# Kernel optimization log

Measured on AMD Instinct MI355X. Metric: run time of the kernel, lower is better.

The kernel has to match this reference:

```python
import jax, jax.numpy as jnp
import numpy as np

D_MODEL = 1024
NUM_HEADS = 16
D_K = D_MODEL // NUM_HEADS


def setup_inputs() -> dict:
    key = jax.random.key(0)
    ks = jax.random.split(key, 11)
    B, T = 4, 2048
    s = 1.0 / np.sqrt(D_MODEL)
    inp = {
        "query": jax.random.normal(ks[0], (B, T, D_MODEL), jnp.float32),
        "key": jax.random.normal(ks[1], (B, T, D_MODEL), jnp.float32),
        "value": jax.random.normal(ks[2], (B, T, D_MODEL), jnp.float32),
        "Wq": jax.random.uniform(ks[3], (D_MODEL, D_MODEL), jnp.float32, -s, s),
        "bq": jax.random.uniform(ks[4], (D_MODEL,), jnp.float32, -s, s),
        "Wk": jax.random.uniform(ks[5], (D_MODEL, D_MODEL), jnp.float32, -s, s),
        "bk": jax.random.uniform(ks[6], (D_MODEL,), jnp.float32, -s, s),
        "Wv": jax.random.uniform(ks[7], (D_MODEL, D_MODEL), jnp.float32, -s, s),
        "bv": jax.random.uniform(ks[8], (D_MODEL,), jnp.float32, -s, s),
        "Wo": jax.random.uniform(ks[9], (D_MODEL, D_MODEL), jnp.float32, -s, s),
        "bo": jax.random.uniform(ks[10], (D_MODEL,), jnp.float32, -s, s),
    }
    return inp


def _split_heads(x):
    B, T, _ = x.shape
    return x.reshape(B, T, NUM_HEADS, D_K).transpose(0, 2, 1, 3)  # (B,H,T,dk)


def reference(query, key, value, Wq, bq, Wk, bk, Wv, bv, Wo, bo):
    q = _split_heads(query @ Wq + bq)   # (B,H,Tq,dk)
    k = _split_heads(key @ Wk + bk)     # (B,H,Tk,dk)
    v = _split_heads(value @ Wv + bv)   # (B,H,Tk,dk)
    scale = 1.0 / jnp.sqrt(jnp.asarray(D_K, q.dtype))
    scores = jnp.einsum("bhqd,bhkd->bhqk", q, k) * scale
    weights = jax.nn.softmax(scores, axis=-1)
    attn = jnp.einsum("bhqk,bhkd->bhqd", weights, v)  # (B,H,Tq,dk)
    B, H, T, dk = attn.shape
    attn = attn.transpose(0, 2, 1, 3).reshape(B, T, H * dk)
    return attn @ Wo + bo
```

## Files before the change

### kernel.cpp

```cpp
#include <hip/hip_runtime.h>
#include <hip/hip_bf16.h>
#include <stdint.h>


typedef __bf16 bf16x8 __attribute__((ext_vector_type(8)));
typedef short  v4s    __attribute__((ext_vector_type(4)));
typedef float  f32x4  __attribute__((ext_vector_type(4)));

#define LOG2E 1.44269504088896340736f

static __device__ __forceinline__ uint32_t f2bf(float x) {
  uint32_t u = __float_as_uint(x);
  u += 0x7fffu + ((u >> 16) & 1u);
  return u >> 16;
}
#if __has_builtin(__builtin_amdgcn_cvt_pk_bf16_f32)
static __device__ __forceinline__ uint32_t pk2bf(float a, float b) {
  typedef __bf16 b2 __attribute__((ext_vector_type(2)));
  union { b2 v; uint32_t u; } x;
  x.v = __builtin_amdgcn_cvt_pk_bf16_f32(a, b);
  return x.u;
}
#else
static __device__ __forceinline__ uint32_t pk2bf(float a, float b) {
  return f2bf(a) | (f2bf(b) << 16);
}
#endif
static __device__ __forceinline__ void gl2lds16(const void* g, void* l) {
  __builtin_amdgcn_global_load_lds(
      (const __attribute__((address_space(1))) uint32_t*)g,
      (__attribute__((address_space(3))) uint32_t*)l, 16, 0, 0);
}

__global__ void convert_inputs(const float* __restrict__ q, const float* __restrict__ k,
                               const float* __restrict__ v, uint16_t* __restrict__ qo,
                               uint16_t* __restrict__ ko, uint16_t* __restrict__ vo) {
  const float* src = blockIdx.y == 0 ? q : (blockIdx.y == 1 ? k : v);
  uint16_t*    dst = blockIdx.y == 0 ? qo : (blockIdx.y == 1 ? ko : vo);
  size_t idx = ((size_t)blockIdx.x * 256 + threadIdx.x) * 8;
  float4 a = *(const float4*)(src + idx);
  float4 b = *(const float4*)(src + idx + 4);
  uint4 o;
  o.x = pk2bf(a.x, a.y); o.y = pk2bf(a.z, a.w);
  o.z = pk2bf(b.x, b.y); o.w = pk2bf(b.z, b.w);
  *(uint4*)(dst + idx) = o;
}

__global__ void transpose_weights(const float* __restrict__ Wq, const float* __restrict__ Wk,
                                  const float* __restrict__ Wv, const float* __restrict__ Wo,
                                  uint16_t* __restrict__ out) {
  __shared__ float t[32][33];
  const float* W = blockIdx.z == 0 ? Wq : blockIdx.z == 1 ? Wk : blockIdx.z == 2 ? Wv : Wo;
  uint16_t* O = out + (size_t)blockIdx.z * 1048576;
  int tx = threadIdx.x & 31, ty = threadIdx.x >> 5;
  int r0 = blockIdx.y * 32, c0 = blockIdx.x * 32;
#pragma unroll
  for (int i = 0; i < 4; i++) t[ty + i * 8][tx] = W[(size_t)(r0 + ty + i * 8) * 1024 + c0 + tx];
  __syncthreads();
#pragma unroll
  for (int i = 0; i < 4; i++)
    O[(size_t)(c0 + ty + i * 8) * 1024 + r0 + tx] = (uint16_t)f2bf(t[tx][ty + i * 8]);
}

static __device__ __forceinline__ void gemm_body(
    const uint16_t* __restrict__ A, const uint16_t* __restrict__ Bt,
    const float* __restrict__ bias, void* __restrict__ Cout,
    int N, int K, int mode, float oscale, int mBase, int nBase,
    uint16_t* __restrict__ lA, uint16_t* __restrict__ lB) {
  int tid = threadIdx.x, wave = tid >> 6, lane = tid & 63;
  int q = lane >> 4, c = lane & 15;
  int wrow = wave & 1, wcol = wave >> 1;
  f32x4 acc[4][4] = {};

  int swz = ((lane & 7) ^ (lane >> 3)) * 8;
  const uint16_t* gA = A + (size_t)(mBase + wave * 32 + (lane >> 3)) * K + swz;
  const uint16_t* gB = Bt + (size_t)(nBase + wave * 32 + (lane >> 3)) * K + swz;
  int cs = c & 7;

  for (int kt = 0; kt < K / 64; kt++) {
    __syncthreads();
    int k0 = kt * 64;
#pragma unroll
    for (int it = 0; it < 4; it++) {
      gl2lds16(gA + (size_t)(it * 8) * K + k0, &lA[(wave * 32 + it * 8) * 64]);
      gl2lds16(gB + (size_t)(it * 8) * K + k0, &lB[(wave * 32 + it * 8) * 64]);
    }
    __syncthreads();
#pragma unroll
    for (int kk = 0; kk < 2; kk++) {
      bf16x8 af[4], bfr[4];
#pragma unroll
      for (int i = 0; i < 4; i++)
        af[i] = *(const bf16x8*)&lA[(wrow * 64 + i * 16 + c) * 64 + ((kk * 4 + q) ^ cs) * 8];
#pragma unroll
      for (int j = 0; j < 4; j++)
        bfr[j] = *(const bf16x8*)&lB[(wcol * 64 + j * 16 + c) * 64 + ((kk * 4 + q) ^ cs) * 8];
#pragma unroll
      for (int i = 0; i < 4; i++)
#pragma unroll
        for (int j = 0; j < 4; j++)
          acc[i][j] = __builtin_amdgcn_mfma_f32_16x16x32_bf16(af[i], bfr[j], acc[i][j], 0, 0, 0);
    }
  }

  float bb[4];
#pragma unroll
  for (int j = 0; j < 4; j++) bb[j] = bias[nBase + wcol * 64 + j * 16 + c];

  if (mode == 0) {
    float* Co = (float*)Cout;
#pragma unroll
    for (int i = 0; i < 4; i++)
#pragma unroll
      for (int j = 0; j < 4; j++) {
        int row = mBase + wrow * 64 + i * 16 + q * 4;
        int col = nBase + wcol * 64 + j * 16 + c;
#pragma unroll
        for (int r = 0; r < 4; r++) Co[(size_t)(row + r) * N + col] = acc[i][j][r] + bb[j];
      }
  } else if (mode == 1) {
    uint16_t* Co = (uint16_t*)Cout;
#pragma unroll
    for (int i = 0; i < 4; i++)
#pragma unroll
      for (int j = 0; j < 4; j++) {
        int row = mBase + wrow * 64 + i * 16 + q * 4;
        int col = nBase + wcol * 64 + j * 16 + c;
#pragma unroll
        for (int r = 0; r < 4; r++)
          Co[(size_t)(row + r) * N + col] = (uint16_t)f2bf((acc[i][j][r] + bb[j]) * oscale);
      }
  } else {
    uint16_t* Co = (uint16_t*)Cout;
#pragma unroll
    for (int i = 0; i < 4; i++)
#pragma unroll
      for (int j = 0; j < 4; j++) {
        int n = nBase + wcol * 64 + j * 16 + c;
        int h = n >> 6, d = n & 63;
        int m = mBase + wrow * 64 + i * 16 + q * 4;
        int b = m >> 11, t = m & 2047;
        uint32_t lo = pk2bf(acc[i][j][0] + bb[j], acc[i][j][1] + bb[j]);
        uint32_t hi = pk2bf(acc[i][j][2] + bb[j], acc[i][j][3] + bb[j]);
        *(uint2*)(Co + (size_t)((b * 16 + h) * 64 + d) * 2048 + t) = make_uint2(lo, hi);
      }
  }
}

__global__ __launch_bounds__(256, 2)
void gemm_qkv(const uint16_t* __restrict__ qb, const uint16_t* __restrict__ kb,
              const uint16_t* __restrict__ vb, const uint16_t* __restrict__ Wtq,
              const uint16_t* __restrict__ Wtk, const uint16_t* __restrict__ Wtv,
              const float* __restrict__ bq, const float* __restrict__ bk,
              const float* __restrict__ bv, uint16_t* __restrict__ Qp,
              uint16_t* __restrict__ Kp, uint16_t* __restrict__ Vt, float cs) {
  __shared__ uint16_t lA[8192], lB[8192];
  int id = blockIdx.x + (blockIdx.y << 3) + (blockIdx.z << 9);
  int xcd = id & 7, j = id >> 3;
  int by = xcd * 8 + (j & 7);
  int bx = (j >> 3) & 7;
  int z  = j >> 6;
  const uint16_t* A  = z == 0 ? qb : (z == 1 ? kb : vb);
  const uint16_t* Bt = z == 0 ? Wtq : (z == 1 ? Wtk : Wtv);
  const float* bias  = z == 0 ? bq : (z == 1 ? bk : bv);
  void* C            = z == 0 ? (void*)Qp : (z == 1 ? (void*)Kp : (void*)Vt);
  int mode   = z == 2 ? 2 : 1;
  float os   = z == 0 ? cs : 1.0f;
  gemm_body(A, Bt, bias, C, 1024, 1024, mode, os, by * 128, bx * 128, lA, lB);
}

__global__ __launch_bounds__(256, 2)
void gemm_out(const uint16_t* __restrict__ A, const uint16_t* __restrict__ Bt,
              const float* __restrict__ bias, float* __restrict__ C) {
  __shared__ uint16_t lA[8192], lB[8192];
  int id = blockIdx.x + (blockIdx.y << 3);
  int xcd = id & 7, j = id >> 3;
  int by = xcd * 8 + (j & 7);
  int bx = j >> 3;
  gemm_body(A, Bt, bias, C, 1024, 1024, 0, 1.0f, by * 128, bx * 128, lA, lB);
}

__global__ __launch_bounds__(256, 2)
void attn(const uint16_t* __restrict__ Qp, const uint16_t* __restrict__ Kp,
          const uint16_t* __restrict__ Vt, uint16_t* __restrict__ Ob) {
  __shared__ uint16_t lds[16384];
  int tid = threadIdx.x, wave = tid >> 6, lane = tid & 63;
  int q = lane >> 4, c = lane & 15;
  int cs = c & 7;
  int gq   = (c & 3) | (((c >> 2) & 1) << 2);
  int rowA = ((c >> 2) << 3) + (c & 3);

  int id = blockIdx.y * 16 + blockIdx.x;
  int wk = (id & 7) * 128 + (id >> 3);
  int qt = wk & 15, bh = wk >> 4;
  int b = bh >> 4, h = bh & 15;
  int qbase = qt * 128;
  int swz = ((lane & 7) ^ (lane >> 3)) * 8;

  {
    const uint16_t* gQ =
        Qp + (size_t)(b * 2048 + qbase + wave * 32 + (lane >> 3)) * 1024 + h * 64 + swz;
#pragma unroll
    for (int it = 0; it < 4; it++)
      gl2lds16(gQ + (size_t)(it * 8) * 1024, &lds[(wave * 32 + it * 8) * 64]);
  }
  __syncthreads();
  bf16x8 qf[2][2];
#pragma unroll
  for (int it = 0; it < 2; it++)
#pragma unroll
    for (int kk = 0; kk < 2; kk++)
      qf[it][kk] =
          *(const bf16x8*)&lds[(wave * 32 + it * 16 + c) * 64 + ((kk * 4 + q) ^ cs) * 8];
  __syncthreads();

  f32x4 o[4][2] = {};
  f32x4 lacc[2] = {};
  union { uint32_t u[4]; bf16x8 v; } one8;
  one8.u[0] = one8.u[1] = one8.u[2] = one8.u[3] = 0x3F803F80u;

  int kchunk = (lane & 7) ^ ((lane >> 3) & 3);
  const uint16_t* gKa =
      Kp + (size_t)(b * 2048 + wave * 16 + (lane >> 3)) * 1024 + h * 64 + kchunk * 8;
  const uint16_t* gKb =
      Kp + (size_t)(b * 2048 + wave * 16 + 8 + (lane >> 3)) * 1024 + h * 64 + (kchunk ^ 4) * 8;
  const uint16_t* gV0 = Vt + (size_t)(bh * 64 + wave * 16 + (lane >> 3)) * 2048 + swz;

  auto stage = [&](int tile, int nb) {
    gl2lds16(gKa + (size_t)(tile * 64) * 1024, &lds[nb + (wave * 16) * 64]);
    gl2lds16(gKb + (size_t)(tile * 64) * 1024, &lds[nb + (wave * 16 + 8) * 64]);
    gl2lds16(gV0 + (size_t)(tile * 64), &lds[8192 + nb + (wave * 16) * 64]);
    gl2lds16(gV0 + (size_t)(8 * 2048) + tile * 64, &lds[8192 + nb + (wave * 16 + 8) * 64]);
  };

  auto compute = [&](const uint16_t* sKc, const uint16_t* sVc) {
    f32x4 s[2][2][2];
#pragma unroll
    for (int p = 0; p < 2; p++) {
      const uint16_t* kr = &sKc[(p * 32 + rowA) * 64];
      bf16x8 aA0 = *(const bf16x8*)&kr[(q ^ gq) * 8];
      bf16x8 aA1 = *(const bf16x8*)&kr[((4 + q) ^ gq) * 8];
      bf16x8 aB0 = *(const bf16x8*)&kr[256 + (q ^ gq) * 8];
      bf16x8 aB1 = *(const bf16x8*)&kr[256 + ((4 + q) ^ gq) * 8];
      s[p][0][0] = __builtin_amdgcn_mfma_f32_16x16x32_bf16(aA0, qf[0][0],
                                                           (f32x4){0.f, 0.f, 0.f, 0.f}, 0, 0, 0);
      s[p][0][0] = __builtin_amdgcn_mfma_f32_16x16x32_bf16(aA1, qf[0][1], s[p][0][0], 0, 0, 0);
      s[p][0][1] = __builtin_amdgcn_mfma_f32_16x16x32_bf16(aA0, qf[1][0],
                                                           (f32x4){0.f, 0.f, 0.f, 0.f}, 0, 0, 0);
      s[p][0][1] = __builtin_amdgcn_mfma_f32_16x16x32_bf16(aA1, qf[1][1], s[p][0][1], 0, 0, 0);
      s[p][1][0] = __builtin_amdgcn_mfma_f32_16x16x32_bf16(aB0, qf[0][0],
                                                           (f32x4){0.f, 0.f, 0.f, 0.f}, 0, 0, 0);
      s[p][1][0] = __builtin_amdgcn_mfma_f32_16x16x32_bf16(aB1, qf[0][1], s[p][1][0], 0, 0, 0);
      s[p][1][1] = __builtin_amdgcn_mfma_f32_16x16x32_bf16(aB0, qf[1][0],
                                                           (f32x4){0.f, 0.f, 0.f, 0.f}, 0, 0, 0);
      s[p][1][1] = __builtin_amdgcn_mfma_f32_16x16x32_bf16(aB1, qf[1][1], s[p][1][1], 0, 0, 0);
    }
#pragma unroll
    for (int p = 0; p < 2; p++) {
      union { uint32_t u[4]; bf16x8 v; } pb[2];
#pragma unroll
      for (int it = 0; it < 2; it++) {
        float a0 = __builtin_amdgcn_exp2f(s[p][0][it][0]);
        float a1 = __builtin_amdgcn_exp2f(s[p][0][it][1]);
        float a2 = __builtin_amdgcn_exp2f(s[p][0][it][2]);
        float a3 = __builtin_amdgcn_exp2f(s[p][0][it][3]);
        float b0 = __builtin_amdgcn_exp2f(s[p][1][it][0]);
        float b1 = __builtin_amdgcn_exp2f(s[p][1][it][1]);
        float b2 = __builtin_amdgcn_exp2f(s[p][1][it][2]);
        float b3 = __builtin_amdgcn_exp2f(s[p][1][it][3]);
        pb[it].u[0] = pk2bf(a0, a1); pb[it].u[1] = pk2bf(a2, a3);
        pb[it].u[2] = pk2bf(b0, b1); pb[it].u[3] = pk2bf(b2, b3);
      }
      lacc[0] = __builtin_amdgcn_mfma_f32_16x16x32_bf16(one8.v, pb[0].v, lacc[0], 0, 0, 0);
      lacc[1] = __builtin_amdgcn_mfma_f32_16x16x32_bf16(one8.v, pb[1].v, lacc[1], 0, 0, 0);
#pragma unroll
      for (int mt = 0; mt < 4; mt++) {
        bf16x8 vv = *(const bf16x8*)&sVc[(mt * 16 + c) * 64 + (((p * 4 + q) ^ cs) * 8)];
        o[mt][0] = __builtin_amdgcn_mfma_f32_16x16x32_bf16(vv, pb[0].v, o[mt][0], 0, 0, 0);
        o[mt][1] = __builtin_amdgcn_mfma_f32_16x16x32_bf16(vv, pb[1].v, o[mt][1], 0, 0, 0);
      }
    }
  };

  stage(0, 0);
  for (int kt2 = 0; kt2 < 16; kt2++) {
    __syncthreads();
    stage(kt2 * 2 + 1, 4096);
    compute(&lds[0], &lds[8192]);
    __syncthreads();
    if (kt2 < 15) stage(kt2 * 2 + 2, 0);
    compute(&lds[4096], &lds[12288]);
  }

  float l[2] = {lacc[0][0], lacc[1][0]};

#pragma unroll
  for (int it = 0; it < 2; it++) {
    float inv = 1.0f / l[it];
    size_t trow = (size_t)(b * 2048 + qbase + wave * 32 + it * 16 + c) * 1024 + h * 64;
#pragma unroll
    for (int mt = 0; mt < 4; mt++) {
      uint32_t lo = pk2bf(o[mt][it][0] * inv, o[mt][it][1] * inv);
      uint32_t hi = pk2bf(o[mt][it][2] * inv, o[mt][it][3] * inv);
      *(uint2*)(Ob + trow + mt * 16 + q * 4) = make_uint2(lo, hi);
    }
  }
}

extern "C" void kernel_launch(void* const* d_in, const int* in_sizes, int n_in,
                              void* d_out, int out_size, void* d_ws, size_t ws_size,
                              hipStream_t stream) {
  (void)in_sizes; (void)n_in; (void)out_size; (void)ws_size;
  const float* query = (const float*)d_in[0];
  const float* key_  = (const float*)d_in[1];
  const float* value = (const float*)d_in[2];
  const float* Wq = (const float*)d_in[3]; const float* bq = (const float*)d_in[4];
  const float* Wk = (const float*)d_in[5]; const float* bk = (const float*)d_in[6];
  const float* Wv = (const float*)d_in[7]; const float* bv = (const float*)d_in[8];
  const float* Wo = (const float*)d_in[9]; const float* bo = (const float*)d_in[10];

  const size_t SZ = (size_t)8192 * 1024;
  uint16_t* buf0 = (uint16_t*)d_ws;
  uint16_t* buf1 = buf0 + SZ;
  uint16_t* buf2 = buf1 + SZ;
  uint16_t* buf3 = buf2 + SZ;
  uint16_t* wts  = buf3 + SZ;
  uint16_t* Wtq = wts;
  uint16_t* Wtk = wts + 1048576;
  uint16_t* Wtv = wts + 2097152;
  uint16_t* Wto = wts + 3145728;
  uint16_t* Kp  = wts + 4194304;
  uint16_t* Vt  = Kp + SZ;

  const float Cs = 0.125f * LOG2E;

  convert_inputs<<<dim3(4096, 3), 256, 0, stream>>>(query, key_, value, buf0, buf1, buf2);
  transpose_weights<<<dim3(32, 32, 4), 256, 0, stream>>>(Wq, Wk, Wv, Wo, wts);
  gemm_qkv<<<dim3(8, 64, 3), 256, 0, stream>>>(buf0, buf1, buf2, Wtq, Wtk, Wtv,
                                               bq, bk, bv, buf3, Kp, Vt, Cs);
  attn<<<dim3(16, 64), 256, 0, stream>>>(buf3, Kp, Vt, buf2);
  gemm_out<<<dim3(8, 64), 256, 0, stream>>>(buf2, Wto, bo, (float*)d_out);
}
```

Before: 329.9 us.

## Fuse fp32-to-bf16 input conversion into QKV GEMM A-tile loads

After: 372.7 us. +13.0%, slower.

```diff
diff --git a/kernel.cpp b/kernel.cpp
--- a/kernel.cpp
+++ b/kernel.cpp
@@ -4,7 +4,6 @@
 
 
 typedef __bf16 bf16x8 __attribute__((ext_vector_type(8)));
-typedef short  v4s    __attribute__((ext_vector_type(4)));
 typedef float  f32x4  __attribute__((ext_vector_type(4)));
 
 #define LOG2E 1.44269504088896340736f
@@ -30,20 +29,6 @@
   __builtin_amdgcn_global_load_lds(
       (const __attribute__((address_space(1))) uint32_t*)g,
       (__attribute__((address_space(3))) uint32_t*)l, 16, 0, 0);
-}
-
-__global__ void convert_inputs(const float* __restrict__ q, const float* __restrict__ k,
-                               const float* __restrict__ v, uint16_t* __restrict__ qo,
-                               uint16_t* __restrict__ ko, uint16_t* __restrict__ vo) {
-  const float* src = blockIdx.y == 0 ? q : (blockIdx.y == 1 ? k : v);
-  uint16_t*    dst = blockIdx.y == 0 ? qo : (blockIdx.y == 1 ? ko : vo);
-  size_t idx = ((size_t)blockIdx.x * 256 + threadIdx.x) * 8;
-  float4 a = *(const float4*)(src + idx);
-  float4 b = *(const float4*)(src + idx + 4);
-  uint4 o;
-  o.x = pk2bf(a.x, a.y); o.y = pk2bf(a.z, a.w);
-  o.z = pk2bf(b.x, b.y); o.w = pk2bf(b.z, b.w);
-  *(uint4*)(dst + idx) = o;
 }
 
 __global__ void transpose_weights(const float* __restrict__ Wq, const float* __restrict__ Wk,
@@ -62,8 +47,9 @@
     O[(size_t)(c0 + ty + i * 8) * 1024 + r0 + tx] = (uint16_t)f2bf(t[tx][ty + i * 8]);
 }
 
+template <bool AF32>
 static __device__ __forceinline__ void gemm_body(
-    const uint16_t* __restrict__ A, const uint16_t* __restrict__ Bt,
+    const void* __restrict__ Ain, const uint16_t* __restrict__ Bt,
     const float* __restrict__ bias, void* __restrict__ Cout,
     int N, int K, int mode, float oscale, int mBase, int nBase,
     uint16_t* __restrict__ lA, uint16_t* __restrict__ lB) {
@@ -72,18 +58,43 @@
   int wrow = wave & 1, wcol = wave >> 1;
   f32x4 acc[4][4] = {};
 
-  int swz = ((lane & 7) ^ (lane >> 3)) * 8;
-  const uint16_t* gA = A + (size_t)(mBase + wave * 32 + (lane >> 3)) * K + swz;
-  const uint16_t* gB = Bt + (size_t)(nBase + wave * 32 + (lane >> 3)) * K + swz;
+  int rho = lane >> 3, j = lane & 7;
+  int swz = (j ^ rho) * 8;
+  const uint16_t* gB  = Bt + (size_t)(nBase + wave * 32 + rho) * K + swz;
+  const uint16_t* gA16 = (const uint16_t*)Ain + (size_t)(mBase + wave * 32 + rho) * K + swz;
+  const float*    gA32 = (const float*)Ain + (size_t)(mBase + wave * 32 + rho) * K + swz;
   int cs = c & 7;
 
   for (int kt = 0; kt < K / 64; kt++) {
     __syncthreads();
     int k0 = kt * 64;
 #pragma unroll
-    for (int it = 0; it < 4; it++) {
-      gl2lds16(gA + (size_t)(it * 8) * K + k0, &lA[(wave * 32 + it * 8) * 64]);
+    for (int it = 0; it < 4; it++)
       gl2lds16(gB + (size_t)(it * 8) * K + k0, &lB[(wave * 32 + it * 8) * 64]);
+    if (AF32) {
+#pragma unroll
+      for (int h2 = 0; h2 < 2; h2++) {
+        float4 fa[2][2];
+#pragma unroll
+        for (int it = 0; it < 2; it++) {
+          const float* p = gA32 + (size_t)((h2 * 2 + it) * 8) * K + k0;
+          fa[it][0] = *(const float4*)p;
+          fa[it][1] = *(const float4*)(p + 4);
+        }
+#pragma unroll
+        for (int it = 0; it < 2; it++) {
+          uint4 ov;
+          ov.x = pk2bf(fa[it][0].x, fa[it][0].y);
+          ov.y = pk2bf(fa[it][0].z, fa[it][0].w);
+          ov.z = pk2bf(fa[it][1].x, fa[it][1].y);
+          ov.w = pk2bf(fa[it][1].z, fa[it][1].w);
+          *(uint4*)&lA[(wave * 32 + (h2 * 2 + it) * 8 + rho) * 64 + j * 8] = ov;
+        }
+      }
+    } else {
+#pragma unroll
+      for (int it = 0; it < 4; it++)
+        gl2lds16(gA16 + (size_t)(it * 8) * K + k0, &lA[(wave * 32 + it * 8) * 64]);
     }
     __syncthreads();
 #pragma unroll
@@ -93,63 +104,63 @@
       for (int i = 0; i < 4; i++)
         af[i] = *(const bf16x8*)&lA[(wrow * 64 + i * 16 + c) * 64 + ((kk * 4 + q) ^ cs) * 8];
 #pragma unroll
-      for (int j = 0; j < 4; j++)
-        bfr[j] = *(const bf16x8*)&lB[(wcol * 64 + j * 16 + c) * 64 + ((kk * 4 + q) ^ cs) * 8];
+      for (int jj = 0; jj < 4; jj++)
+        bfr[jj] = *(const bf16x8*)&lB[(wcol * 64 + jj * 16 + c) * 64 + ((kk * 4 + q) ^ cs) * 8];
 #pragma unroll
       for (int i = 0; i < 4; i++)
 #pragma unroll
-        for (int j = 0; j < 4; j++)
-          acc[i][j] = __builtin_amdgcn_mfma_f32_16x16x32_bf16(af[i], bfr[j], acc[i][j], 0, 0, 0);
+        for (int jj = 0; jj < 4; jj++)
+          acc[i][jj] = __builtin_amdgcn_mfma_f32_16x16x32_bf16(af[i], bfr[jj], acc[i][jj], 0, 0, 0);
     }
   }
 
   float bb[4];
 #pragma unroll
-  for (int j = 0; j < 4; j++) bb[j] = bias[nBase + wcol * 64 + j * 16 + c];
+  for (int jj = 0; jj < 4; jj++) bb[jj] = bias[nBase + wcol * 64 + jj * 16 + c];
 
   if (mode == 0) {
     float* Co = (float*)Cout;
 #pragma unroll
     for (int i = 0; i < 4; i++)
 #pragma unroll
-      for (int j = 0; j < 4; j++) {
+      for (int jj = 0; jj < 4; jj++) {
         int row = mBase + wrow * 64 + i * 16 + q * 4;
-        int col = nBase + wcol * 64 + j * 16 + c;
-#pragma unroll
-        for (int r = 0; r < 4; r++) Co[(size_t)(row + r) * N + col] = acc[i][j][r] + bb[j];
+        int col = nBase + wcol * 64 + jj * 16 + c;
+#pragma unroll
+        for (int r = 0; r < 4; r++) Co[(size_t)(row + r) * N + col] = acc[i][jj][r] + bb[jj];
       }
   } else if (mode == 1) {
     uint16_t* Co = (uint16_t*)Cout;
 #pragma unroll
     for (int i = 0; i < 4; i++)
 #pragma unroll
-      for (int j = 0; j < 4; j++) {
+      for (int jj = 0; jj < 4; jj++) {
         int row = mBase + wrow * 64 + i * 16 + q * 4;
-        int col = nBase + wcol * 64 + j * 16 + c;
+        int col = nBase + wcol * 64 + jj * 16 + c;
 #pragma unroll
         for (int r = 0; r < 4; r++)
-          Co[(size_t)(row + r) * N + col] = (uint16_t)f2bf((acc[i][j][r] + bb[j]) * oscale);
+          Co[(size_t)(row + r) * N + col] = (uint16_t)f2bf((acc[i][jj][r] + bb[jj]) * oscale);
       }
   } else {
     uint16_t* Co = (uint16_t*)Cout;
 #pragma unroll
     for (int i = 0; i < 4; i++)
 #pragma unroll
-      for (int j = 0; j < 4; j++) {
-        int n = nBase + wcol * 64 + j * 16 + c;
+      for (int jj = 0; jj < 4; jj++) {
+        int n = nBase + wcol * 64 + jj * 16 + c;
         int h = n >> 6, d = n & 63;
         int m = mBase + wrow * 64 + i * 16 + q * 4;
         int b = m >> 11, t = m & 2047;
-        uint32_t lo = pk2bf(acc[i][j][0] + bb[j], acc[i][j][1] + bb[j]);
-        uint32_t hi = pk2bf(acc[i][j][2] + bb[j], acc[i][j][3] + bb[j]);
+        uint32_t lo = pk2bf(acc[i][jj][0] + bb[jj], acc[i][jj][1] + bb[jj]);
+        uint32_t hi = pk2bf(acc[i][jj][2] + bb[jj], acc[i][jj][3] + bb[jj]);
         *(uint2*)(Co + (size_t)((b * 16 + h) * 64 + d) * 2048 + t) = make_uint2(lo, hi);
       }
   }
 }
 
 __global__ __launch_bounds__(256, 2)
-void gemm_qkv(const uint16_t* __restrict__ qb, const uint16_t* __restrict__ kb,
-              const uint16_t* __restrict__ vb, const uint16_t* __restrict__ Wtq,
+void gemm_qkv(const float* __restrict__ qs, const float* __restrict__ ks,
+              const float* __restrict__ vs, const uint16_t* __restrict__ Wtq,
               const uint16_t* __restrict__ Wtk, const uint16_t* __restrict__ Wtv,
               const float* __restrict__ bq, const float* __restrict__ bk,
               const float* __restrict__ bv, uint16_t* __restrict__ Qp,
@@ -157,16 +168,16 @@
   __shared__ uint16_t lA[8192], lB[8192];
   int id = blockIdx.x + (blockIdx.y << 3) + (blockIdx.z << 9);
   int xcd = id & 7, j = id >> 3;
-  int by = xcd * 8 + (j & 7);
-  int bx = (j >> 3) & 7;
+  int bx = j & 7;
+  int by = xcd * 8 + ((j >> 3) & 7);
   int z  = j >> 6;
-  const uint16_t* A  = z == 0 ? qb : (z == 1 ? kb : vb);
+  const void* A      = z == 0 ? (const void*)qs : (z == 1 ? (const void*)ks : (const void*)vs);
   const uint16_t* Bt = z == 0 ? Wtq : (z == 1 ? Wtk : Wtv);
   const float* bias  = z == 0 ? bq : (z == 1 ? bk : bv);
   void* C            = z == 0 ? (void*)Qp : (z == 1 ? (void*)Kp : (void*)Vt);
   int mode   = z == 2 ? 2 : 1;
   float os   = z == 0 ? cs : 1.0f;
-  gemm_body(A, Bt, bias, C, 1024, 1024, mode, os, by * 128, bx * 128, lA, lB);
+  gemm_body<true>(A, Bt, bias, C, 1024, 1024, mode, os, by * 128, bx * 128, lA, lB);
 }
 
 __global__ __launch_bounds__(256, 2)
@@ -175,9 +186,9 @@
   __shared__ uint16_t lA[8192], lB[8192];
   int id = blockIdx.x + (blockIdx.y << 3);
   int xcd = id & 7, j = id >> 3;
-  int by = xcd * 8 + (j & 7);
-  int bx = j >> 3;
-  gemm_body(A, Bt, bias, C, 1024, 1024, 0, 1.0f, by * 128, bx * 128, lA, lB);
+  int bx = j & 7;
+  int by = xcd * 8 + (j >> 3);
+  gemm_body<false>(A, Bt, bias, C, 1024, 1024, 0, 1.0f, by * 128, bx * 128, lA, lB);
 }
 
 __global__ __launch_bounds__(256, 2)
@@ -334,9 +345,8 @@
 
   const float Cs = 0.125f * LOG2E;
 
-  convert_inputs<<<dim3(4096, 3), 256, 0, stream>>>(query, key_, value, buf0, buf1, buf2);
   transpose_weights<<<dim3(32, 32, 4), 256, 0, stream>>>(Wq, Wk, Wv, Wo, wts);
-  gemm_qkv<<<dim3(8, 64, 3), 256, 0, stream>>>(buf0, buf1, buf2, Wtq, Wtk, Wtv,
+  gemm_qkv<<<dim3(8, 64, 3), 256, 0, stream>>>(query, key_, value, Wtq, Wtk, Wtv,
                                                bq, bk, bv, buf3, Kp, Vt, Cs);
   attn<<<dim3(16, 64), 256, 0, stream>>>(buf3, Kp, Vt, buf2);
   gemm_out<<<dim3(8, 64), 256, 0, stream>>>(buf2, Wto, bo, (float*)d_out);
```
